# Kernel optimization log

Hardware: AMD Instinct MI355X
Metric: run time of the kernel (lower is better)

The kernel has to match this reference:

```python
import jax, jax.numpy as jnp
import numpy as np

S = 16384          # number of ragged segments (ranking lists)
AVG_LEN = 512      # average list length
N = S * AVG_LEN    # total elements = 8,388,608


def setup_inputs() -> dict:
    key = jax.random.key(0)
    k1, k2 = jax.random.split(key)
    rng = np.random.default_rng(0)
    lengths = rng.integers(128, 897, size=S)
    # force exact total so concatenated tensors have a fixed shape N
    lengths[-1] += N - lengths.sum()
    scope = jnp.asarray(lengths, dtype=jnp.int32)
    means = jax.random.normal(k1, (N,), dtype=jnp.float32)
    targets_train = jax.random.normal(k2, (N,), dtype=jnp.float32)
    return {"means": means, "scope": scope, "targets_train": targets_train}


def reference(means, scope, targets_train):
    num_seg = scope.shape[0]
    n = means.shape[0]
    # segment id for every element, from ragged lengths (jit-safe: fixed total)
    seg = jnp.repeat(jnp.arange(num_seg, dtype=jnp.int32), scope,
                     total_repeat_length=n)
    # per-segment softmax of targets (stable)
    tmax = jax.ops.segment_max(targets_train, seg, num_segments=num_seg)
    te = jnp.exp(targets_train - tmax[seg])
    tden = jax.ops.segment_sum(te, seg, num_segments=num_seg)
    p = te / tden[seg]
    # per-segment log_softmax of means (stable)
    mmax = jax.ops.segment_max(means, seg, num_segments=num_seg)
    shifted = means - mmax[seg]
    lse = jnp.log(jax.ops.segment_sum(jnp.exp(shifted), seg, num_segments=num_seg))
    logq = shifted - lse[seg]
    # sum of per-segment cross-entropies, averaged over segments
    loss = -jnp.sum(p * logq)
    return loss / num_seg
```

## Files before the change

kernel.cpp:

```cpp
#include <hip/hip_runtime.h>
#include <hip/hip_bf16.h>

#define BLK_T 256
#define SEGS_PER_BLK 16
#define SEGS_PER_WAVE 4

__global__ __launch_bounds__(BLK_T)
void fused_seg_loss(const float* __restrict__ means,
                    const float* __restrict__ targets,
                    const int* __restrict__ scope,
                    float* __restrict__ blockLoss, int S) {
    __shared__ int   sOff[SEGS_PER_BLK];
    __shared__ int   sLen[SEGS_PER_BLK];
    __shared__ int   sPart[4];
    __shared__ float sWave[4];

    int b    = blockIdx.x;
    int tid  = threadIdx.x;
    int lane = tid & 63;
    int wv   = tid >> 6;
    int first = b * SEGS_PER_BLK;
    int nseg  = S - first; if (nseg > SEGS_PER_BLK) nseg = SEGS_PER_BLK;

    int part = 0;
    const int4* sp4 = (const int4*)scope;
    int n4 = first >> 2;
    for (int i = tid; i < n4; i += BLK_T) {
        int4 v = sp4[i];
        part += (v.x + v.y) + (v.z + v.w);
    }
#pragma unroll
    for (int o = 32; o > 0; o >>= 1) part += __shfl_xor(part, o, 64);
    if (lane == 0) sPart[wv] = part;
    __syncthreads();

    if (tid == 0) {
        int base = (sPart[0] + sPart[1]) + (sPart[2] + sPart[3]);
        for (int i = 0; i < nseg; ++i) {
            int L = scope[first + i];
            sOff[i] = base; sLen[i] = L; base += L;
        }
    }
    __syncthreads();

    float td[SEGS_PER_WAVE], md[SEGS_PER_WAVE], Av[SEGS_PER_WAVE];
#pragma unroll
    for (int q = 0; q < SEGS_PER_WAVE; ++q) {
        int si = (wv << 2) + q;
        float tden = 0.f, mden = 0.f, A = 0.f;
        if (si < nseg && sLen[si] > 0) {
            int start = sOff[si], len = sLen[si];
            const float* __restrict__ T = targets + start;
            const float* __restrict__ M = means + start;
            int head = (4 - (start & 3)) & 3; if (head > len) head = len;
            int nv    = (len - head) >> 2;
            int tailb = head + (nv << 2);
            int tail  = len - tailb;
            const float4* __restrict__ T4 = (const float4*)(T + head);
            const float4* __restrict__ M4 = (const float4*)(M + head);

            if (lane < head) {
                float t = T[lane], m = M[lane];
                float e = __expf(t);
                tden += e; mden += __expf(m); A += e * m;
            }
            if (lane < tail) {
                float t = T[tailb + lane], m = M[tailb + lane];
                float e = __expf(t);
                tden += e; mden += __expf(m); A += e * m;
            }
            int v = lane;
            for (; v + 64 < nv; v += 128) {
                float4 a = T4[v], bb = T4[v + 64];
                float4 c = M4[v], d  = M4[v + 64];
                float e0 = __expf(a.x), e1 = __expf(a.y), e2 = __expf(a.z), e3 = __expf(a.w);
                float e4 = __expf(bb.x), e5 = __expf(bb.y), e6 = __expf(bb.z), e7 = __expf(bb.w);
                tden += ((e0 + e1) + (e2 + e3)) + ((e4 + e5) + (e6 + e7));
                mden += ((__expf(c.x) + __expf(c.y)) + (__expf(c.z) + __expf(c.w)))
                      + ((__expf(d.x) + __expf(d.y)) + (__expf(d.z) + __expf(d.w)));
                A    += ((e0 * c.x + e1 * c.y) + (e2 * c.z + e3 * c.w))
                      + ((e4 * d.x + e5 * d.y) + (e6 * d.z + e7 * d.w));
            }
            for (; v < nv; v += 64) {
                float4 a = T4[v], c = M4[v];
                float e0 = __expf(a.x), e1 = __expf(a.y), e2 = __expf(a.z), e3 = __expf(a.w);
                tden += (e0 + e1) + (e2 + e3);
                mden += (__expf(c.x) + __expf(c.y)) + (__expf(c.z) + __expf(c.w));
                A    += (e0 * c.x + e1 * c.y) + (e2 * c.z + e3 * c.w);
            }
        }
        td[q] = tden; md[q] = mden; Av[q] = A;
    }

#pragma unroll
    for (int o = 32; o > 0; o >>= 1) {
#pragma unroll
        for (int q = 0; q < SEGS_PER_WAVE; ++q) {
            td[q] += __shfl_xor(td[q], o, 64);
            md[q] += __shfl_xor(md[q], o, 64);
            Av[q] += __shfl_xor(Av[q], o, 64);
        }
    }

    if (lane == 0) {
        float loss = 0.f;
#pragma unroll
        for (int q = 0; q < SEGS_PER_WAVE; ++q) {
            int si = (wv << 2) + q;
            if (si < nseg && sLen[si] > 0)
                loss += logf(md[q]) - Av[q] / td[q];
        }
        sWave[wv] = loss;
    }
    __syncthreads();
    if (tid == 0)
        blockLoss[b] = (sWave[0] + sWave[1]) + (sWave[2] + sWave[3]);
}

__global__ __launch_bounds__(BLK_T)
void final_reduce(const float* __restrict__ blockLoss,
                  float* __restrict__ out, int nb, int S) {
    __shared__ float w[4];
    int tid = threadIdx.x, lane = tid & 63, wv = tid >> 6;
    float s = 0.f;
    for (int i = tid; i < nb; i += BLK_T) s += blockLoss[i];
#pragma unroll
    for (int o = 32; o > 0; o >>= 1) s += __shfl_xor(s, o, 64);
    if (lane == 0) w[wv] = s;
    __syncthreads();
    if (tid == 0) out[0] = ((w[0] + w[1]) + (w[2] + w[3])) / (float)S;
}

extern "C" void kernel_launch(void* const* d_in, const int* in_sizes, int n_in,
                              void* d_out, int out_size, void* d_ws, size_t ws_size,
                              hipStream_t stream) {
    const float* means   = (const float*)d_in[0];
    const int*   scope   = (const int*)d_in[1];
    const float* targets = (const float*)d_in[2];
    int S = in_sizes[1];
    float* out = (float*)d_out;

    float* blockLoss = (float*)d_ws;
    int nb = (S + SEGS_PER_BLK - 1) / SEGS_PER_BLK;

    fused_seg_loss<<<nb, BLK_T, 0, stream>>>(means, targets, scope, blockLoss, S);
    final_reduce<<<1, BLK_T, 0, stream>>>(blockLoss, out, nb, S);
}
```

Before: 30.43 us.

## Interleave four segments per wave loop and parallelize segment offset scan

Each wave now iterates over its four segments together in one loop, issuing loads for all four before computing, to raise memory-level parallelism and avoid serial per-segment loops with short tails. The serial single-thread offset computation is replaced by a wave-level shuffle prefix scan. Launch bounds add a minimum-occupancy hint. The cost is more live registers and predicated work when segment lengths differ.

```diff
diff --git a/kernel.cpp b/kernel.cpp
--- a/kernel.cpp
+++ b/kernel.cpp
@@ -5,7 +5,7 @@
 #define SEGS_PER_BLK 16
 #define SEGS_PER_WAVE 4
 
-__global__ __launch_bounds__(BLK_T)
+__global__ __launch_bounds__(BLK_T, 4)
 void fused_seg_loss(const float* __restrict__ means,
                     const float* __restrict__ targets,
                     const int* __restrict__ scope,
@@ -34,62 +34,90 @@
     if (lane == 0) sPart[wv] = part;
     __syncthreads();
 
-    if (tid == 0) {
+    if (wv == 0) {
         int base = (sPart[0] + sPart[1]) + (sPart[2] + sPart[3]);
-        for (int i = 0; i < nseg; ++i) {
-            int L = scope[first + i];
-            sOff[i] = base; sLen[i] = L; base += L;
+        int L = (lane < nseg) ? scope[first + lane] : 0;
+        int inc = L;
+#pragma unroll
+        for (int o = 1; o < 16; o <<= 1) {
+            int v = __shfl_up(inc, o, 64);
+            if (lane >= o) inc += v;
         }
+        if (lane < SEGS_PER_BLK) { sOff[lane] = base + inc - L; sLen[lane] = L; }
     }
     __syncthreads();
 
-    float td[SEGS_PER_WAVE], md[SEGS_PER_WAVE], Av[SEGS_PER_WAVE];
+    float td[SEGS_PER_WAVE] = {0.f, 0.f, 0.f, 0.f};
+    float md[SEGS_PER_WAVE] = {0.f, 0.f, 0.f, 0.f};
+    float Av[SEGS_PER_WAVE] = {0.f, 0.f, 0.f, 0.f};
+    const float4* T4[SEGS_PER_WAVE];
+    const float4* M4[SEGS_PER_WAVE];
+    int nv[SEGS_PER_WAVE];
+    int maxnv = 0;
+
 #pragma unroll
     for (int q = 0; q < SEGS_PER_WAVE; ++q) {
         int si = (wv << 2) + q;
-        float tden = 0.f, mden = 0.f, A = 0.f;
-        if (si < nseg && sLen[si] > 0) {
-            int start = sOff[si], len = sLen[si];
-            const float* __restrict__ T = targets + start;
-            const float* __restrict__ M = means + start;
+        int start = 0, len = 0;
+        if (si < nseg) { start = sOff[si]; len = sLen[si]; }
+        if (len <= 0) {
+            nv[q] = 0;
+            T4[q] = (const float4*)means; M4[q] = (const float4*)means;
+        } else {
+            const float* T = targets + start;
+            const float* M = means + start;
             int head = (4 - (start & 3)) & 3; if (head > len) head = len;
-            int nv    = (len - head) >> 2;
-            int tailb = head + (nv << 2);
+            int n     = (len - head) >> 2;
+            int tailb = head + (n << 2);
             int tail  = len - tailb;
-            const float4* __restrict__ T4 = (const float4*)(T + head);
-            const float4* __restrict__ M4 = (const float4*)(M + head);
-
+            T4[q] = (const float4*)(T + head);
+            M4[q] = (const float4*)(M + head);
+            nv[q] = n; if (n > maxnv) maxnv = n;
             if (lane < head) {
                 float t = T[lane], m = M[lane];
                 float e = __expf(t);
-                tden += e; mden += __expf(m); A += e * m;
+                td[q] += e; md[q] += __expf(m); Av[q] += e * m;
             }
             if (lane < tail) {
                 float t = T[tailb + lane], m = M[tailb + lane];
                 float e = __expf(t);
-                tden += e; mden += __expf(m); A += e * m;
-            }
-            int v = lane;
-            for (; v + 64 < nv; v += 128) {
-                float4 a = T4[v], bb = T4[v + 64];
-                float4 c = M4[v], d  = M4[v + 64];
-                float e0 = __expf(a.x), e1 = __expf(a.y), e2 = __expf(a.z), e3 = __expf(a.w);
-                float e4 = __expf(bb.x), e5 = __expf(bb.y), e6 = __expf(bb.z), e7 = __expf(bb.w);
-                tden += ((e0 + e1) + (e2 + e3)) + ((e4 + e5) + (e6 + e7));
-                mden += ((__expf(c.x) + __expf(c.y)) + (__expf(c.z) + __expf(c.w)))
-                      + ((__expf(d.x) + __expf(d.y)) + (__expf(d.z) + __expf(d.w)));
-                A    += ((e0 * c.x + e1 * c.y) + (e2 * c.z + e3 * c.w))
-                      + ((e4 * d.x + e5 * d.y) + (e6 * d.z + e7 * d.w));
-            }
-            for (; v < nv; v += 64) {
-                float4 a = T4[v], c = M4[v];
-                float e0 = __expf(a.x), e1 = __expf(a.y), e2 = __expf(a.z), e3 = __expf(a.w);
-                tden += (e0 + e1) + (e2 + e3);
-                mden += (__expf(c.x) + __expf(c.y)) + (__expf(c.z) + __expf(c.w));
-                A    += (e0 * c.x + e1 * c.y) + (e2 * c.z + e3 * c.w);
+                td[q] += e; md[q] += __expf(m); Av[q] += e * m;
             }
         }
-        td[q] = tden; md[q] = mden; Av[q] = A;
+    }
+
+    for (int rbase = 0; rbase < maxnv; rbase += 64) {
+        float4 a0, a1, a2, a3, c0, c1, c2, c3;
+        int v = rbase + lane;
+        bool x0 = v < nv[0], x1 = v < nv[1], x2 = v < nv[2], x3 = v < nv[3];
+        if (x0) { a0 = T4[0][v]; c0 = M4[0][v]; }
+        if (x1) { a1 = T4[1][v]; c1 = M4[1][v]; }
+        if (x2) { a2 = T4[2][v]; c2 = M4[2][v]; }
+        if (x3) { a3 = T4[3][v]; c3 = M4[3][v]; }
+        if (x0) {
+            float e0 = __expf(a0.x), e1 = __expf(a0.y), e2 = __expf(a0.z), e3 = __expf(a0.w);
+            td[0] += (e0 + e1) + (e2 + e3);
+            md[0] += (__expf(c0.x) + __expf(c0.y)) + (__expf(c0.z) + __expf(c0.w));
+            Av[0] += (e0 * c0.x + e1 * c0.y) + (e2 * c0.z + e3 * c0.w);
+        }
+        if (x1) {
+            float e0 = __expf(a1.x), e1 = __expf(a1.y), e2 = __expf(a1.z), e3 = __expf(a1.w);
+            td[1] += (e0 + e1) + (e2 + e3);
+            md[1] += (__expf(c1.x) + __expf(c1.y)) + (__expf(c1.z) + __expf(c1.w));
+            Av[1] += (e0 * c1.x + e1 * c1.y) + (e2 * c1.z + e3 * c1.w);
+        }
+        if (x2) {
+            float e0 = __expf(a2.x), e1 = __expf(a2.y), e2 = __expf(a2.z), e3 = __expf(a2.w);
+            td[2] += (e0 + e1) + (e2 + e3);
+            md[2] += (__expf(c2.x) + __expf(c2.y)) + (__expf(c2.z) + __expf(c2.w));
+            Av[2] += (e0 * c2.x + e1 * c2.y) + (e2 * c2.z + e3 * c2.w);
+        }
+        if (x3) {
+            float e0 = __expf(a3.x), e1 = __expf(a3.y), e2 = __expf(a3.z), e3 = __expf(a3.w);
+            td[3] += (e0 + e1) + (e2 + e3);
+            md[3] += (__expf(c3.x) + __expf(c3.y)) + (__expf(c3.z) + __expf(c3.w));
+            Av[3] += (e0 * c3.x + e1 * c3.y) + (e2 * c3.z + e3 * c3.w);
+        }
     }
 
 #pragma unroll
@@ -107,7 +135,7 @@
 #pragma unroll
         for (int q = 0; q < SEGS_PER_WAVE; ++q) {
             int si = (wv << 2) + q;
-            if (si < nseg && sLen[si] > 0)
+            if (si < nseg && nv[q] >= 0 && sLen[si] > 0)
                 loss += logf(md[q]) - Av[q] / td[q];
         }
         sWave[wv] = loss;
```

Result: slower. 49.50 us (+62.6%).

## Assign one segment per wave and write per-segment losses for final reduce

Applied to the files above, without the earlier changes.

Cuts segments per block from 16 to 4 so each wave handles a single segment, which quadruples the grid and removes the serial four-segment loop per wave. Segment offsets within a block are now computed with a wave shuffle scan instead of a single-thread loop. The final reduce now sums per-segment losses with 1024 threads, using a float4 fast path when S is 16384. The trade-off is that every block still re-sums the scope prefix, so four times as many blocks means more redundant scope reads.

```diff
diff --git a/kernel.cpp b/kernel.cpp
--- a/kernel.cpp
+++ b/kernel.cpp
@@ -2,18 +2,16 @@
 #include <hip/hip_bf16.h>
 
 #define BLK_T 256
-#define SEGS_PER_BLK 16
-#define SEGS_PER_WAVE 4
+#define SEGS_PER_BLK 4
 
 __global__ __launch_bounds__(BLK_T)
 void fused_seg_loss(const float* __restrict__ means,
                     const float* __restrict__ targets,
                     const int* __restrict__ scope,
-                    float* __restrict__ blockLoss, int S) {
-    __shared__ int   sOff[SEGS_PER_BLK];
-    __shared__ int   sLen[SEGS_PER_BLK];
-    __shared__ int   sPart[4];
-    __shared__ float sWave[4];
+                    float* __restrict__ segl, int S) {
+    __shared__ int sPart[4];
+    __shared__ int sOff[SEGS_PER_BLK];
+    __shared__ int sLen[SEGS_PER_BLK];
 
     int b    = blockIdx.x;
     int tid  = threadIdx.x;
@@ -21,6 +19,7 @@
     int wv   = tid >> 6;
     int first = b * SEGS_PER_BLK;
     int nseg  = S - first; if (nseg > SEGS_PER_BLK) nseg = SEGS_PER_BLK;
+    if (nseg <= 0) return;
 
     int part = 0;
     const int4* sp4 = (const int4*)scope;
@@ -34,101 +33,100 @@
     if (lane == 0) sPart[wv] = part;
     __syncthreads();
 
-    if (tid == 0) {
+    if (wv == 0) {
         int base = (sPart[0] + sPart[1]) + (sPart[2] + sPart[3]);
-        for (int i = 0; i < nseg; ++i) {
-            int L = scope[first + i];
-            sOff[i] = base; sLen[i] = L; base += L;
+        int L = (lane < nseg) ? scope[first + lane] : 0;
+        int inc = L;
+#pragma unroll
+        for (int o = 1; o < 4; o <<= 1) {
+            int v = __shfl_up(inc, o, 64);
+            if (lane >= o) inc += v;
         }
+        if (lane < SEGS_PER_BLK) { sOff[lane] = base + inc - L; sLen[lane] = L; }
     }
     __syncthreads();
 
-    float td[SEGS_PER_WAVE], md[SEGS_PER_WAVE], Av[SEGS_PER_WAVE];
-#pragma unroll
-    for (int q = 0; q < SEGS_PER_WAVE; ++q) {
-        int si = (wv << 2) + q;
-        float tden = 0.f, mden = 0.f, A = 0.f;
-        if (si < nseg && sLen[si] > 0) {
-            int start = sOff[si], len = sLen[si];
-            const float* __restrict__ T = targets + start;
-            const float* __restrict__ M = means + start;
-            int head = (4 - (start & 3)) & 3; if (head > len) head = len;
-            int nv    = (len - head) >> 2;
-            int tailb = head + (nv << 2);
-            int tail  = len - tailb;
-            const float4* __restrict__ T4 = (const float4*)(T + head);
-            const float4* __restrict__ M4 = (const float4*)(M + head);
+    if (wv >= nseg) return;
+    int start = sOff[wv];
+    int len   = sLen[wv];
+    if (len <= 0) { if (lane == 0) segl[first + wv] = 0.f; return; }
 
-            if (lane < head) {
-                float t = T[lane], m = M[lane];
-                float e = __expf(t);
-                tden += e; mden += __expf(m); A += e * m;
-            }
-            if (lane < tail) {
-                float t = T[tailb + lane], m = M[tailb + lane];
-                float e = __expf(t);
-                tden += e; mden += __expf(m); A += e * m;
-            }
-            int v = lane;
-            for (; v + 64 < nv; v += 128) {
-                float4 a = T4[v], bb = T4[v + 64];
-                float4 c = M4[v], d  = M4[v + 64];
-                float e0 = __expf(a.x), e1 = __expf(a.y), e2 = __expf(a.z), e3 = __expf(a.w);
-                float e4 = __expf(bb.x), e5 = __expf(bb.y), e6 = __expf(bb.z), e7 = __expf(bb.w);
-                tden += ((e0 + e1) + (e2 + e3)) + ((e4 + e5) + (e6 + e7));
-                mden += ((__expf(c.x) + __expf(c.y)) + (__expf(c.z) + __expf(c.w)))
-                      + ((__expf(d.x) + __expf(d.y)) + (__expf(d.z) + __expf(d.w)));
-                A    += ((e0 * c.x + e1 * c.y) + (e2 * c.z + e3 * c.w))
-                      + ((e4 * d.x + e5 * d.y) + (e6 * d.z + e7 * d.w));
-            }
-            for (; v < nv; v += 64) {
-                float4 a = T4[v], c = M4[v];
-                float e0 = __expf(a.x), e1 = __expf(a.y), e2 = __expf(a.z), e3 = __expf(a.w);
-                tden += (e0 + e1) + (e2 + e3);
-                mden += (__expf(c.x) + __expf(c.y)) + (__expf(c.z) + __expf(c.w));
-                A    += (e0 * c.x + e1 * c.y) + (e2 * c.z + e3 * c.w);
-            }
-        }
-        td[q] = tden; md[q] = mden; Av[q] = A;
+    const float* __restrict__ T = targets + start;
+    const float* __restrict__ M = means + start;
+    int head = (4 - (start & 3)) & 3; if (head > len) head = len;
+    int nv    = (len - head) >> 2;
+    int tailb = head + (nv << 2);
+    int tail  = len - tailb;
+    const float4* __restrict__ T4 = (const float4*)(T + head);
+    const float4* __restrict__ M4 = (const float4*)(M + head);
+
+    float tden = 0.f, mden = 0.f, A = 0.f;
+
+    if (lane < head) {
+        float t = T[lane], m = M[lane];
+        float e = __expf(t);
+        tden += e; mden += __expf(m); A += e * m;
+    }
+    if (lane < tail) {
+        float t = T[tailb + lane], m = M[tailb + lane];
+        float e = __expf(t);
+        tden += e; mden += __expf(m); A += e * m;
+    }
+
+    int v = lane;
+    for (; v + 64 < nv; v += 128) {
+        float4 a = T4[v], bb = T4[v + 64];
+        float4 c = M4[v], d  = M4[v + 64];
+        float e0 = __expf(a.x), e1 = __expf(a.y), e2 = __expf(a.z), e3 = __expf(a.w);
+        float e4 = __expf(bb.x), e5 = __expf(bb.y), e6 = __expf(bb.z), e7 = __expf(bb.w);
+        tden += ((e0 + e1) + (e2 + e3)) + ((e4 + e5) + (e6 + e7));
+        mden += ((__expf(c.x) + __expf(c.y)) + (__expf(c.z) + __expf(c.w)))
+              + ((__expf(d.x) + __expf(d.y)) + (__expf(d.z) + __expf(d.w)));
+        A    += ((e0 * c.x + e1 * c.y) + (e2 * c.z + e3 * c.w))
+              + ((e4 * d.x + e5 * d.y) + (e6 * d.z + e7 * d.w));
+    }
+    for (; v < nv; v += 64) {
+        float4 a = T4[v], c = M4[v];
+        float e0 = __expf(a.x), e1 = __expf(a.y), e2 = __expf(a.z), e3 = __expf(a.w);
+        tden += (e0 + e1) + (e2 + e3);
+        mden += (__expf(c.x) + __expf(c.y)) + (__expf(c.z) + __expf(c.w));
+        A    += (e0 * c.x + e1 * c.y) + (e2 * c.z + e3 * c.w);
     }
 
 #pragma unroll
     for (int o = 32; o > 0; o >>= 1) {
-#pragma unroll
-        for (int q = 0; q < SEGS_PER_WAVE; ++q) {
-            td[q] += __shfl_xor(td[q], o, 64);
-            md[q] += __shfl_xor(md[q], o, 64);
-            Av[q] += __shfl_xor(Av[q], o, 64);
-        }
+        tden += __shfl_xor(tden, o, 64);
+        mden += __shfl_xor(mden, o, 64);
+        A    += __shfl_xor(A,    o, 64);
     }
-
-    if (lane == 0) {
-        float loss = 0.f;
-#pragma unroll
-        for (int q = 0; q < SEGS_PER_WAVE; ++q) {
-            int si = (wv << 2) + q;
-            if (si < nseg && sLen[si] > 0)
-                loss += logf(md[q]) - Av[q] / td[q];
-        }
-        sWave[wv] = loss;
-    }
-    __syncthreads();
-    if (tid == 0)
-        blockLoss[b] = (sWave[0] + sWave[1]) + (sWave[2] + sWave[3]);
+    if (lane == 0) segl[first + wv] = logf(mden) - A / tden;
 }
 
-__global__ __launch_bounds__(BLK_T)
-void final_reduce(const float* __restrict__ blockLoss,
-                  float* __restrict__ out, int nb, int S) {
-    __shared__ float w[4];
-    int tid = threadIdx.x, lane = tid & 63, wv = tid >> 6;
+__global__ __launch_bounds__(1024)
+void final_reduce(const float* __restrict__ segl,
+                  float* __restrict__ out, int S) {
+    __shared__ float wsum[16];
+    int tid = threadIdx.x;
     float s = 0.f;
-    for (int i = tid; i < nb; i += BLK_T) s += blockLoss[i];
+    if (S == 16384) {
+        const float4* p = (const float4*)(segl + tid * 16);
+        float4 a = p[0], b = p[1], c = p[2], d = p[3];
+        s = ((a.x + a.y) + (a.z + a.w)) + ((b.x + b.y) + (b.z + b.w))
+          + ((c.x + c.y) + (c.z + c.w)) + ((d.x + d.y) + (d.z + d.w));
+    } else {
+        for (int i = tid; i < S; i += 1024) s += segl[i];
+    }
 #pragma unroll
-    for (int o = 32; o > 0; o >>= 1) s += __shfl_xor(s, o, 64);
-    if (lane == 0) w[wv] = s;
+    for (int o = 32; o > 0; o >>= 1) s += __shfl_down(s, o, 64);
+    int lane = tid & 63, wave = tid >> 6;
+    if (lane == 0) wsum[wave] = s;
     __syncthreads();
-    if (tid == 0) out[0] = ((w[0] + w[1]) + (w[2] + w[3])) / (float)S;
+    if (tid == 0) {
+        float tot = 0.f;
+#pragma unroll
+        for (int w = 0; w < 16; ++w) tot += wsum[w];
+        out[0] = tot / (float)S;
+    }
 }
 
 extern "C" void kernel_launch(void* const* d_in, const int* in_sizes, int n_in,
@@ -140,9 +138,9 @@
     int S = in_sizes[1];
     float* out = (float*)d_out;
 
-    float* blockLoss = (float*)d_ws;
+    float* segl = (float*)d_ws;
     int nb = (S + SEGS_PER_BLK - 1) / SEGS_PER_BLK;
 
-    fused_seg_loss<<<nb, BLK_T, 0, stream>>>(means, targets, scope, blockLoss, S);
-    final_reduce<<<1, BLK_T, 0, stream>>>(blockLoss, out, nb, S);
+    fused_seg_loss<<<nb, BLK_T, 0, stream>>>(means, targets, scope, segl, S);
+    final_reduce<<<1, 1024, 0, stream>>>(segl, out, S);
 }
```

After: 32.60 us. 7.1% more time.

## Assign one segment per wave in 1024-thread blocks with a parallel offset scan

Applied to the files above, without the earlier changes.

Blocks grow to 1024 threads so each of the 16 waves handles a single segment, instead of 4 waves each looping over 4 segments one after another. The serial thread-0 loop that built segment offsets is replaced by a wave-level shuffle scan. The per-block prefix read of scope is unrolled into four clamped int4 loads. The final reduce gains a float4 fast path for 1024 partials. The unrolled prefix loads silently assume at most 4096 int4 chunks before a block, which ties correctness to the current problem size.

```diff
diff --git a/kernel.cpp b/kernel.cpp
--- a/kernel.cpp
+++ b/kernel.cpp
@@ -1,19 +1,18 @@
 #include <hip/hip_runtime.h>
 #include <hip/hip_bf16.h>
 
-#define BLK_T 256
+#define BLK_T 1024
 #define SEGS_PER_BLK 16
-#define SEGS_PER_WAVE 4
 
 __global__ __launch_bounds__(BLK_T)
 void fused_seg_loss(const float* __restrict__ means,
                     const float* __restrict__ targets,
                     const int* __restrict__ scope,
                     float* __restrict__ blockLoss, int S) {
+    __shared__ int   sPart[16];
     __shared__ int   sOff[SEGS_PER_BLK];
     __shared__ int   sLen[SEGS_PER_BLK];
-    __shared__ int   sPart[4];
-    __shared__ float sWave[4];
+    __shared__ float sWave[SEGS_PER_BLK];
 
     int b    = blockIdx.x;
     int tid  = threadIdx.x;
@@ -21,109 +20,122 @@
     int wv   = tid >> 6;
     int first = b * SEGS_PER_BLK;
     int nseg  = S - first; if (nseg > SEGS_PER_BLK) nseg = SEGS_PER_BLK;
+    if (nseg <= 0) return;
 
     int part = 0;
-    const int4* sp4 = (const int4*)scope;
     int n4 = first >> 2;
-    for (int i = tid; i < n4; i += BLK_T) {
-        int4 v = sp4[i];
-        part += (v.x + v.y) + (v.z + v.w);
+    if (n4 > 0) {
+        const int4* sp4 = (const int4*)scope;
+        int c  = n4 - 1;
+        int i0 = tid;
+        int i1 = tid + 1024;
+        int i2 = tid + 2048;
+        int i3 = tid + 3072;
+        int4 v0 = sp4[min(i0, c)];
+        int4 v1 = sp4[min(i1, c)];
+        int4 v2 = sp4[min(i2, c)];
+        int4 v3 = sp4[min(i3, c)];
+        if (i0 < n4) part += (v0.x + v0.y) + (v0.z + v0.w);
+        if (i1 < n4) part += (v1.x + v1.y) + (v1.z + v1.w);
+        if (i2 < n4) part += (v2.x + v2.y) + (v2.z + v2.w);
+        if (i3 < n4) part += (v3.x + v3.y) + (v3.z + v3.w);
     }
 #pragma unroll
     for (int o = 32; o > 0; o >>= 1) part += __shfl_xor(part, o, 64);
     if (lane == 0) sPart[wv] = part;
     __syncthreads();
 
-    if (tid == 0) {
-        int base = (sPart[0] + sPart[1]) + (sPart[2] + sPart[3]);
-        for (int i = 0; i < nseg; ++i) {
-            int L = scope[first + i];
-            sOff[i] = base; sLen[i] = L; base += L;
+    if (wv == 0) {
+        int p = (lane < 16) ? sPart[lane] : 0;
+        int L = (lane < 16 && lane < nseg) ? scope[first + lane] : 0;
+        int tot = p;
+#pragma unroll
+        for (int o = 8; o > 0; o >>= 1) tot += __shfl_xor(tot, o, 64);
+        int inc = L;
+#pragma unroll
+        for (int o = 1; o < 16; o <<= 1) {
+            int v = __shfl_up(inc, o, 64);
+            if (lane >= o) inc += v;
         }
+        if (lane < SEGS_PER_BLK) { sOff[lane] = tot + inc - L; sLen[lane] = L; }
     }
     __syncthreads();
 
-    float td[SEGS_PER_WAVE], md[SEGS_PER_WAVE], Av[SEGS_PER_WAVE];
+    float loss = 0.f;
+    bool valid = (wv < nseg) && (sLen[wv] > 0);
+    if (valid) {
+        int start = sOff[wv];
+        int len   = sLen[wv];
+        const float* __restrict__ T = targets + start;
+        const float* __restrict__ M = means + start;
+        int head = (4 - (start & 3)) & 3; if (head > len) head = len;
+        int nv    = (len - head) >> 2;
+        int tailb = head + (nv << 2);
+        int tail  = len - tailb;
+        const float4* __restrict__ T4 = (const float4*)(T + head);
+        const float4* __restrict__ M4 = (const float4*)(M + head);
+
+        float tden = 0.f, mden = 0.f, A = 0.f;
+        if (lane < head) {
+            float t = T[lane], m = M[lane];
+            float e = __expf(t);
+            tden += e; mden += __expf(m); A += e * m;
+        }
+        if (lane < tail) {
+            float t = T[tailb + lane], m = M[tailb + lane];
+            float e = __expf(t);
+            tden += e; mden += __expf(m); A += e * m;
+        }
+        int v = lane;
+        for (; v + 64 < nv; v += 128) {
+            float4 a = T4[v], bb = T4[v + 64];
+            float4 c = M4[v], d  = M4[v + 64];
+            float e0 = __expf(a.x), e1 = __expf(a.y), e2 = __expf(a.z), e3 = __expf(a.w);
+            float e4 = __expf(bb.x), e5 = __expf(bb.y), e6 = __expf(bb.z), e7 = __expf(bb.w);
+            tden += ((e0 + e1) + (e2 + e3)) + ((e4 + e5) + (e6 + e7));
+            mden += ((__expf(c.x) + __expf(c.y)) + (__expf(c.z) + __expf(c.w)))
+                  + ((__expf(d.x) + __expf(d.y)) + (__expf(d.z) + __expf(d.w)));
+            A    += ((e0 * c.x + e1 * c.y) + (e2 * c.z + e3 * c.w))
+                  + ((e4 * d.x + e5 * d.y) + (e6 * d.z + e7 * d.w));
+        }
+        for (; v < nv; v += 64) {
+            float4 a = T4[v], c = M4[v];
+            float e0 = __expf(a.x), e1 = __expf(a.y), e2 = __expf(a.z), e3 = __expf(a.w);
+            tden += (e0 + e1) + (e2 + e3);
+            mden += (__expf(c.x) + __expf(c.y)) + (__expf(c.z) + __expf(c.w));
+            A    += (e0 * c.x + e1 * c.y) + (e2 * c.z + e3 * c.w);
+        }
 #pragma unroll
-    for (int q = 0; q < SEGS_PER_WAVE; ++q) {
-        int si = (wv << 2) + q;
-        float tden = 0.f, mden = 0.f, A = 0.f;
-        if (si < nseg && sLen[si] > 0) {
-            int start = sOff[si], len = sLen[si];
-            const float* __restrict__ T = targets + start;
-            const float* __restrict__ M = means + start;
-            int head = (4 - (start & 3)) & 3; if (head > len) head = len;
-            int nv    = (len - head) >> 2;
-            int tailb = head + (nv << 2);
-            int tail  = len - tailb;
-            const float4* __restrict__ T4 = (const float4*)(T + head);
-            const float4* __restrict__ M4 = (const float4*)(M + head);
-
-            if (lane < head) {
-                float t = T[lane], m = M[lane];
-                float e = __expf(t);
-                tden += e; mden += __expf(m); A += e * m;
-            }
-            if (lane < tail) {
-                float t = T[tailb + lane], m = M[tailb + lane];
-                float e = __expf(t);
-                tden += e; mden += __expf(m); A += e * m;
-            }
-            int v = lane;
-            for (; v + 64 < nv; v += 128) {
-                float4 a = T4[v], bb = T4[v + 64];
-                float4 c = M4[v], d  = M4[v + 64];
-                float e0 = __expf(a.x), e1 = __expf(a.y), e2 = __expf(a.z), e3 = __expf(a.w);
-                float e4 = __expf(bb.x), e5 = __expf(bb.y), e6 = __expf(bb.z), e7 = __expf(bb.w);
-                tden += ((e0 + e1) + (e2 + e3)) + ((e4 + e5) + (e6 + e7));
-                mden += ((__expf(c.x) + __expf(c.y)) + (__expf(c.z) + __expf(c.w)))
-                      + ((__expf(d.x) + __expf(d.y)) + (__expf(d.z) + __expf(d.w)));
-                A    += ((e0 * c.x + e1 * c.y) + (e2 * c.z + e3 * c.w))
-                      + ((e4 * d.x + e5 * d.y) + (e6 * d.z + e7 * d.w));
-            }
-            for (; v < nv; v += 64) {
-                float4 a = T4[v], c = M4[v];
-                float e0 = __expf(a.x), e1 = __expf(a.y), e2 = __expf(a.z), e3 = __expf(a.w);
-                tden += (e0 + e1) + (e2 + e3);
-                mden += (__expf(c.x) + __expf(c.y)) + (__expf(c.z) + __expf(c.w));
-                A    += (e0 * c.x + e1 * c.y) + (e2 * c.z + e3 * c.w);
-            }
+        for (int o = 32; o > 0; o >>= 1) {
+            tden += __shfl_xor(tden, o, 64);
+            mden += __shfl_xor(mden, o, 64);
+            A    += __shfl_xor(A,    o, 64);
         }
-        td[q] = tden; md[q] = mden; Av[q] = A;
+        loss = logf(mden) - A / tden;
     }
 
+    if (lane == 0) sWave[wv] = valid ? loss : 0.f;
+    __syncthreads();
+    if (tid == 0) {
+        float s = 0.f;
 #pragma unroll
-    for (int o = 32; o > 0; o >>= 1) {
-#pragma unroll
-        for (int q = 0; q < SEGS_PER_WAVE; ++q) {
-            td[q] += __shfl_xor(td[q], o, 64);
-            md[q] += __shfl_xor(md[q], o, 64);
-            Av[q] += __shfl_xor(Av[q], o, 64);
-        }
+        for (int w = 0; w < SEGS_PER_BLK; ++w) s += sWave[w];
+        blockLoss[b] = s;
     }
-
-    if (lane == 0) {
-        float loss = 0.f;
-#pragma unroll
-        for (int q = 0; q < SEGS_PER_WAVE; ++q) {
-            int si = (wv << 2) + q;
-            if (si < nseg && sLen[si] > 0)
-                loss += logf(md[q]) - Av[q] / td[q];
-        }
-        sWave[wv] = loss;
-    }
-    __syncthreads();
-    if (tid == 0)
-        blockLoss[b] = (sWave[0] + sWave[1]) + (sWave[2] + sWave[3]);
 }
 
-__global__ __launch_bounds__(BLK_T)
+__global__ __launch_bounds__(256)
 void final_reduce(const float* __restrict__ blockLoss,
                   float* __restrict__ out, int nb, int S) {
     __shared__ float w[4];
     int tid = threadIdx.x, lane = tid & 63, wv = tid >> 6;
     float s = 0.f;
-    for (int i = tid; i < nb; i += BLK_T) s += blockLoss[i];
+    if (nb == 1024) {
+        float4 a = ((const float4*)blockLoss)[tid];
+        s = (a.x + a.y) + (a.z + a.w);
+    } else {
+        for (int i = tid; i < nb; i += 256) s += blockLoss[i];
+    }
 #pragma unroll
     for (int o = 32; o > 0; o >>= 1) s += __shfl_xor(s, o, 64);
     if (lane == 0) w[wv] = s;
@@ -144,5 +156,5 @@
     int nb = (S + SEGS_PER_BLK - 1) / SEGS_PER_BLK;
 
     fused_seg_loss<<<nb, BLK_T, 0, stream>>>(means, targets, scope, blockLoss, S);
-    final_reduce<<<1, BLK_T, 0, stream>>>(blockLoss, out, nb, S);
+    final_reduce<<<1, 256, 0, stream>>>(blockLoss, out, nb, S);
 }
```

New measurement: 30.58 us. Within noise of the previous version (+0.5%).
